# Performance work log

Hardware: AMD Instinct MI355X
Metric: run time of the kernel (lower is better)

## Reference

```python
import jax, jax.numpy as jnp
import numpy as np

N, E, F_IN, H, R = 50000, 1600000, 770, 64, 3


def _lin_params(key, fan_in, fan_out, scale=0.02):
    return jax.random.normal(key, (fan_in, fan_out), dtype=jnp.float32) * scale


def setup_inputs() -> dict:
    key = jax.random.key(0)
    ks = jax.random.split(key, 20)
    x = jax.random.normal(ks[0], (N, F_IN), dtype=jnp.float32)
    edge_index = jax.random.randint(ks[1], (2, E), 0, N, dtype=jnp.int64)
    edge_type = jax.random.randint(ks[2], (E,), 0, R, dtype=jnp.int64)
    # RGCN layer params: W [R, fin, H], root [fin, H], bias [H]
    W1 = jax.random.normal(ks[3], (R, F_IN, H), dtype=jnp.float32) * 0.02
    root1 = _lin_params(ks[4], F_IN, H)
    b1 = jnp.zeros((H,), jnp.float32)
    W2 = jax.random.normal(ks[5], (R, H, H), dtype=jnp.float32) * 0.02
    root2 = _lin_params(ks[6], H, H)
    b2 = jnp.zeros((H,), jnp.float32)
    W3 = jax.random.normal(ks[7], (R, H, H), dtype=jnp.float32) * 0.02
    root3 = _lin_params(ks[8], H, H)
    b3 = jnp.zeros((H,), jnp.float32)
    ln_g = jnp.ones((H,), jnp.float32)
    ln_b = jnp.zeros((H,), jnp.float32)
    ew1 = _lin_params(ks[9], 2 * H, H)
    eb1 = jnp.zeros((H,), jnp.float32)
    ew2 = _lin_params(ks[10], H, 3)
    eb2 = jnp.zeros((3,), jnp.float32)
    nw1 = _lin_params(ks[11], H, H // 2)
    nb1 = jnp.zeros((H // 2,), jnp.float32)
    nw2 = _lin_params(ks[12], H // 2, 2)
    nb2 = jnp.zeros((2,), jnp.float32)
    return dict(x=x, edge_index=edge_index, edge_type=edge_type,
                W1=W1, root1=root1, b1=b1, W2=W2, root2=root2, b2=b2,
                W3=W3, root3=root3, b3=b3, ln_g=ln_g, ln_b=ln_b,
                ew1=ew1, eb1=eb1, ew2=ew2, eb2=eb2,
                nw1=nw1, nb1=nb1, nw2=nw2, nb2=nb2)


def rgcn_conv(x, W, root, bias, row, col, etype):
    # per-relation transform of all nodes: [R, N, H]
    xr = jnp.einsum('nf,rfh->rnh', x, W)
    msg = xr[etype, row]                       # [E, H] gather
    seg = etype * N + col                      # combined (relation, dst) key
    sums = jax.ops.segment_sum(msg, seg, num_segments=R * N)
    cnt = jax.ops.segment_sum(jnp.ones((msg.shape[0],), msg.dtype), seg,
                              num_segments=R * N)
    mean = sums / jnp.maximum(cnt, 1.0)[:, None]   # mean aggr per relation
    agg = mean.reshape(R, N, -1).sum(0)
    return agg + x @ root + bias


def layer_norm(x, g, b, eps=1e-5):
    mu = x.mean(-1, keepdims=True)
    var = ((x - mu) ** 2).mean(-1, keepdims=True)
    return (x - mu) * jax.lax.rsqrt(var + eps) * g + b


def reference(x, edge_index, edge_type, W1, root1, b1, W2, root2, b2,
              W3, root3, b3, ln_g, ln_b, ew1, eb1, ew2, eb2,
              nw1, nb1, nw2, nb2):
    row, col = edge_index[0], edge_index[1]
    x1 = jax.nn.relu(rgcn_conv(x, W1, root1, b1, row, col, edge_type))
    x2 = jax.nn.relu(rgcn_conv(x1, W2, root2, b2, row, col, edge_type))
    x3 = layer_norm(rgcn_conv(x2, W3, root3, b3, row, col, edge_type), ln_g, ln_b)
    # edge classifier on concatenated endpoint features (dropout = identity in eval)
    ef = jnp.concatenate([x3[row], x3[col]], axis=-1)    # [E, 2H]
    eh = jax.nn.relu(ef @ ew1 + eb1)
    edge_out = jax.nn.log_softmax(eh @ ew2 + eb2, axis=-1)
    nh = jax.nn.relu(x3 @ nw1 + nb1)
    node_out = jax.nn.log_softmax(nh @ nw2 + nb2, axis=-1)
    return edge_out, node_out
```

## Files before the change

kernel.cpp:

```cpp
#include <hip/hip_runtime.h>
#include <hip/hip_bf16.h>
#include <math.h>

#define Nn 50000
#define Ee 1600000
#define RR 3
#define RN (RR * Nn)
#define FIN 770
#define KPAD1 800

typedef __attribute__((ext_vector_type(8))) short short8;
typedef __attribute__((ext_vector_type(4))) float floatx4;

static __device__ __forceinline__ unsigned short f2bf(float v) {
  __hip_bfloat16 h = __float2bfloat16(v);
  return *(unsigned short*)&h;
}

__global__ __launch_bounds__(256) void count_kernel(const int* __restrict__ ei,
                                                    const int* __restrict__ et,
                                                    int* __restrict__ counts,
                                                    int* __restrict__ rank) {
  int e = blockIdx.x * 256 + threadIdx.x;
  if (e >= Ee) return;
  int col = ei[Ee + e];
  int r = et[e];
  rank[e] = atomicAdd(&counts[r * Nn + col], 1);
}

__global__ __launch_bounds__(256) void scan1_kernel(const int* __restrict__ counts,
                                                    int* __restrict__ offs,
                                                    int* __restrict__ bsums, int n) {
  __shared__ int sh[256];
  int t = threadIdx.x;
  int base = blockIdx.x * 1024 + t * 4;
  int v0 = (base + 0 < n) ? counts[base + 0] : 0;
  int v1 = (base + 1 < n) ? counts[base + 1] : 0;
  int v2 = (base + 2 < n) ? counts[base + 2] : 0;
  int v3 = (base + 3 < n) ? counts[base + 3] : 0;
  int tot = v0 + v1 + v2 + v3;
  sh[t] = tot;
  __syncthreads();
  for (int off = 1; off < 256; off <<= 1) {
    int v = (t >= off) ? sh[t - off] : 0;
    __syncthreads();
    sh[t] += v;
    __syncthreads();
  }
  int run = sh[t] - tot;
  if (base + 0 < n) offs[base + 0] = run; run += v0;
  if (base + 1 < n) offs[base + 1] = run; run += v1;
  if (base + 2 < n) offs[base + 2] = run; run += v2;
  if (base + 3 < n) offs[base + 3] = run;
  if (t == 255) bsums[blockIdx.x] = sh[255];
}

__global__ __launch_bounds__(256) void scan_top_kernel(int* __restrict__ bsums, int nb) {
  __shared__ int sh[256];
  int t = threadIdx.x;
  int v = (t < nb) ? bsums[t] : 0;
  sh[t] = v;
  __syncthreads();
  for (int off = 1; off < 256; off <<= 1) {
    int x = (t >= off) ? sh[t - off] : 0;
    __syncthreads();
    sh[t] += x;
    __syncthreads();
  }
  if (t < nb) bsums[t] = sh[t] - v;
}

__global__ __launch_bounds__(256) void scan_add_kernel(int* __restrict__ offs,
                                                       const int* __restrict__ bsums,
                                                       int n) {
  int i = blockIdx.x * 256 + threadIdx.x;
  if (i > n) return;
  if (i == n) { offs[n] = Ee; return; }
  offs[i] += bsums[i >> 10];
}

__global__ __launch_bounds__(256) void fill_kernel(const int* __restrict__ ei,
                                                   const int* __restrict__ et,
                                                   const int* __restrict__ offs,
                                                   const int* __restrict__ rank,
                                                   int* __restrict__ srcs) {
  int e = blockIdx.x * 256 + threadIdx.x;
  if (e >= Ee) return;
  int row = ei[e];
  int col = ei[Ee + e];
  int r = et[e];
  int s = r * Nn + col;
  srcs[offs[s] + rank[e]] = row;
}

__global__ __launch_bounds__(256) void prep_wt_kernel(const float* __restrict__ W,
                                                      const float* __restrict__ root,
                                                      unsigned short* __restrict__ Wt,
                                                      int K, int Kpad) {
  int i = blockIdx.x * 256 + threadIdx.x;
  if (i >= 256 * Kpad) return;
  int c = i / Kpad, k = i % Kpad;
  float v = 0.f;
  if (k < K) {
    if (c < 192) {
      int r = c >> 6, h = c & 63;
      v = W[((long)r * K + k) * 64 + h];
    } else {
      v = root[k * 64 + (c - 192)];
    }
  }
  Wt[i] = f2bf(v);
}

__global__ __launch_bounds__(256) void prep_wth_kernel(const float* __restrict__ ew1,
                                                       const float* __restrict__ eb1,
                                                       unsigned short* __restrict__ Wth,
                                                       float* __restrict__ biasH) {
  int i = blockIdx.x * 256 + threadIdx.x;
  if (i < 128) biasH[i] = (i < 64) ? eb1[i] : 0.f;
  if (i >= 256 * 64) return;
  int c = i >> 6, k = i & 63;
  float v = 0.f;
  if (c < 64) v = ew1[k * 64 + c];
  else if (c < 128) v = ew1[(64 + k) * 64 + (c - 64)];
  Wth[i] = f2bf(v);
}

#define ASTR 40
#define BSTR 40

#define LOAD_A_FULL(k0)                                        \
  {                                                            \
    const float* ap = aRow + (k0) + ac;                        \
    a01 = *(const float4*)(ap + 0);                            \
    a23 = *(const float4*)(ap + 4);                            \
  }
#define LOAD_A_MASK(k0)                                        \
  {                                                            \
    int kb = (k0) + ac;                                        \
    a01.x = (rowOK && kb + 0 < K) ? aRow[kb + 0] : 0.f;        \
    a01.y = (rowOK && kb + 1 < K) ? aRow[kb + 1] : 0.f;        \
    a01.z = (rowOK && kb + 2 < K) ? aRow[kb + 2] : 0.f;        \
    a01.w = (rowOK && kb + 3 < K) ? aRow[kb + 3] : 0.f;        \
    a23.x = (rowOK && kb + 4 < K) ? aRow[kb + 4] : 0.f;        \
    a23.y = (rowOK && kb + 5 < K) ? aRow[kb + 5] : 0.f;        \
    a23.z = (rowOK && kb + 6 < K) ? aRow[kb + 6] : 0.f;        \
    a23.w = (rowOK && kb + 7 < K) ? aRow[kb + 7] : 0.f;        \
  }
#define LOAD_A(k0)                                                   \
  {                                                                  \
    if (aBf16) { aB = *(const int4*)(aRowB + (k0) + ac); }           \
    else if (rowOK && (k0) + 32 <= K) LOAD_A_FULL(k0)                \
    else LOAD_A_MASK(k0)                                             \
  }
#define LOAD_B(k0)                                             \
  {                                                            \
    b0 = *(const int4*)(wRow + (k0));                          \
  }
#define STORE_TILE()                                                          \
  {                                                                           \
    if (aBf16) {                                                              \
      *(int4*)&As[ar * ASTR + ac] = aB;                                       \
    } else {                                                                  \
      __hip_bfloat162* adst = (__hip_bfloat162*)&As[ar * ASTR + ac];          \
      adst[0] = __hip_bfloat162(__float2bfloat16(a01.x), __float2bfloat16(a01.y)); \
      adst[1] = __hip_bfloat162(__float2bfloat16(a01.z), __float2bfloat16(a01.w)); \
      adst[2] = __hip_bfloat162(__float2bfloat16(a23.x), __float2bfloat16(a23.y)); \
      adst[3] = __hip_bfloat162(__float2bfloat16(a23.z), __float2bfloat16(a23.w)); \
    }                                                                         \
    *(int4*)&Bs[br * BSTR + bo] = b0;                                         \
  }

__global__ __launch_bounds__(1024) void gemm_bf16_kernel(
    const void* __restrict__ Ag, const unsigned short* __restrict__ Wt,
    unsigned short* __restrict__ Cg, const float* __restrict__ bias,
    int M, int K, int Kpad, int Ncol, int aBf16) {
  __shared__ unsigned short As[256 * ASTR];
  __shared__ unsigned short Bs[256 * BSTR];
  int t = threadIdx.x;
  int lane = t & 63;
  int wid = t >> 6;
  int quad = lane >> 4;
  int l16 = lane & 15;
  int rowBase = blockIdx.x * 256;
  int mbase = (wid >> 2) * 64;
  int nbase = (wid & 3) * 64;

  floatx4 acc[4][4];
#pragma unroll
  for (int i = 0; i < 4; ++i)
#pragma unroll
    for (int j = 0; j < 4; ++j) acc[i][j] = (floatx4){0.f, 0.f, 0.f, 0.f};

  int ar = t >> 2;
  int ac = (t & 3) * 8;
  long gm = rowBase + ar;
  bool rowOK = (gm < M);
  const float* aRow = (const float*)Ag + gm * (long)K;
  const unsigned short* aRowB = (const unsigned short*)Ag + gm * (long)K;
  int br = t >> 2;
  int bo = (t & 3) * 8;
  const unsigned short* wRow = Wt + (size_t)br * Kpad + bo;

  float4 a01, a23;
  int4 aB;
  int4 b0;

  int KT = Kpad / 32;
  LOAD_A(0);
  LOAD_B(0);

  for (int kt = 0; kt < KT; ++kt) {
    STORE_TILE();
    __syncthreads();

    if (kt + 1 < KT) {
      int k0n = (kt + 1) * 32;
      LOAD_A(k0n);
      LOAD_B(k0n);
    }

    short8 af[4], bfr[4];
#pragma unroll
    for (int i = 0; i < 4; ++i)
      af[i] = *(const short8*)&As[(mbase + i * 16 + l16) * ASTR + quad * 8];
#pragma unroll
    for (int j = 0; j < 4; ++j)
      bfr[j] = *(const short8*)&Bs[(nbase + j * 16 + l16) * BSTR + quad * 8];

#pragma unroll
    for (int i = 0; i < 4; ++i)
#pragma unroll
      for (int j = 0; j < 4; ++j)
        acc[i][j] = __builtin_amdgcn_mfma_f32_16x16x32_bf16(af[i], bfr[j], acc[i][j], 0, 0, 0);
    __syncthreads();
  }

#pragma unroll
  for (int j = 0; j < 4; ++j) {
    int gn = nbase + j * 16 + l16;
    if (gn >= Ncol) continue;
    float bv = bias ? bias[gn] : 0.f;
#pragma unroll
    for (int i = 0; i < 4; ++i) {
      int gm0 = rowBase + mbase + i * 16 + quad * 4;
#pragma unroll
      for (int r = 0; r < 4; ++r) {
        int gmm = gm0 + r;
        if (gmm < M) Cg[(long)gmm * Ncol + gn] = f2bf(acc[i][j][r] + bv);
      }
    }
  }
}

#define AGG_RESOLVE(ii, ee, vv, rr)                                   \
  {                                                                   \
    if ((ii) < c0)       { ee = b0 + (ii);         vv = inv0; rr = 0; }   \
    else if ((ii) < c01) { ee = b1 + ((ii) - c0);  vv = inv1; rr = 64; }  \
    else                 { ee = b2 + ((ii) - c01); vv = inv2; rr = 128; } \
  }
#define AGG_FMA8(v, inv)                                              \
  {                                                                   \
    unsigned u0 = (unsigned)v.x, u1 = (unsigned)v.y;                  \
    unsigned u2 = (unsigned)v.z, u3 = (unsigned)v.w;                  \
    a0 = fmaf(__int_as_float(u0 << 16), inv, a0);                     \
    a1 = fmaf(__int_as_float(u0 & 0xffff0000u), inv, a1);             \
    a2 = fmaf(__int_as_float(u1 << 16), inv, a2);                     \
    a3 = fmaf(__int_as_float(u1 & 0xffff0000u), inv, a3);             \
    a4 = fmaf(__int_as_float(u2 << 16), inv, a4);                     \
    a5 = fmaf(__int_as_float(u2 & 0xffff0000u), inv, a5);             \
    a6 = fmaf(__int_as_float(u3 << 16), inv, a6);                     \
    a7 = fmaf(__int_as_float(u3 & 0xffff0000u), inv, a7);             \
  }

__global__ __launch_bounds__(256) void agg_kernel(const unsigned short* __restrict__ XR,
                                                  const int* __restrict__ offs,
                                                  const int* __restrict__ srcs,
                                                  const float* __restrict__ bias,
                                                  const float* __restrict__ lng,
                                                  const float* __restrict__ lnb,
                                                  float* __restrict__ out, int mode) {
  int lane = threadIdx.x & 63;
  int wid = threadIdx.x >> 6;
  int slot = lane >> 3;
  int l8 = lane & 7;
  int dst = blockIdx.x * 4 + wid;
  if (dst >= Nn) return;

  int b0 = offs[dst],          e0 = offs[dst + 1];
  int b1 = offs[Nn + dst],     e1 = offs[Nn + dst + 1];
  int b2 = offs[2 * Nn + dst], e2 = offs[2 * Nn + dst + 1];
  int c0 = e0 - b0, c1 = e1 - b1, c2 = e2 - b2;
  int c01 = c0 + c1;
  int tot = c01 + c2;
  float inv0 = (c0 > 0) ? 1.f / (float)c0 : 0.f;
  float inv1 = (c1 > 0) ? 1.f / (float)c1 : 0.f;
  float inv2 = (c2 > 0) ? 1.f / (float)c2 : 0.f;

  float a0 = 0.f, a1 = 0.f, a2 = 0.f, a3 = 0.f;
  float a4 = 0.f, a5 = 0.f, a6 = 0.f, a7 = 0.f;
  for (int i = slot; i < tot; i += 16) {
    int ea; float iva; int ra;
    AGG_RESOLVE(i, ea, iva, ra);
    int ib = i + 8;
    int eb; float ivb; int rb;
    if (ib < tot) { AGG_RESOLVE(ib, eb, ivb, rb); }
    else          { eb = ea; ivb = 0.f; rb = ra; }
    int sa = srcs[ea];
    int sb = srcs[eb];
    int4 va = *(const int4*)&XR[(long)sa * 256 + ra + l8 * 8];
    int4 vb = *(const int4*)&XR[(long)sb * 256 + rb + l8 * 8];
    AGG_FMA8(va, iva);
    AGG_FMA8(vb, ivb);
  }
#pragma unroll
  for (int m = 8; m < 64; m <<= 1) {
    a0 += __shfl_xor(a0, m, 64); a1 += __shfl_xor(a1, m, 64);
    a2 += __shfl_xor(a2, m, 64); a3 += __shfl_xor(a3, m, 64);
    a4 += __shfl_xor(a4, m, 64); a5 += __shfl_xor(a5, m, 64);
    a6 += __shfl_xor(a6, m, 64); a7 += __shfl_xor(a7, m, 64);
  }

  int4 rt = *(const int4*)&XR[(long)dst * 256 + 192 + l8 * 8];
  unsigned r0 = (unsigned)rt.x, r1 = (unsigned)rt.y;
  unsigned r2 = (unsigned)rt.z, r3 = (unsigned)rt.w;
  float4 bv0 = *(const float4*)&bias[l8 * 8];
  float4 bv1 = *(const float4*)&bias[l8 * 8 + 4];
  float t0 = a0 + __int_as_float(r0 << 16) + bv0.x;
  float t1 = a1 + __int_as_float(r0 & 0xffff0000u) + bv0.y;
  float t2 = a2 + __int_as_float(r1 << 16) + bv0.z;
  float t3 = a3 + __int_as_float(r1 & 0xffff0000u) + bv0.w;
  float t4 = a4 + __int_as_float(r2 << 16) + bv1.x;
  float t5 = a5 + __int_as_float(r2 & 0xffff0000u) + bv1.y;
  float t6 = a6 + __int_as_float(r3 << 16) + bv1.z;
  float t7 = a7 + __int_as_float(r3 & 0xffff0000u) + bv1.w;

  if (mode == 0) {
    if (slot == 0) {
      unsigned short* outB = (unsigned short*)out;
      int4 o;
      o.x = (int)((unsigned)f2bf(fmaxf(t0, 0.f)) | ((unsigned)f2bf(fmaxf(t1, 0.f)) << 16));
      o.y = (int)((unsigned)f2bf(fmaxf(t2, 0.f)) | ((unsigned)f2bf(fmaxf(t3, 0.f)) << 16));
      o.z = (int)((unsigned)f2bf(fmaxf(t4, 0.f)) | ((unsigned)f2bf(fmaxf(t5, 0.f)) << 16));
      o.w = (int)((unsigned)f2bf(fmaxf(t6, 0.f)) | ((unsigned)f2bf(fmaxf(t7, 0.f)) << 16));
      *(int4*)&outB[(long)dst * 64 + l8 * 8] = o;
    }
  } else {
    float s = t0 + t1 + t2 + t3 + t4 + t5 + t6 + t7;
    s += __shfl_xor(s, 1, 64); s += __shfl_xor(s, 2, 64); s += __shfl_xor(s, 4, 64);
    float mu = s * (1.f / 64.f);
    float d0 = t0 - mu, d1 = t1 - mu, d2 = t2 - mu, d3 = t3 - mu;
    float d4 = t4 - mu, d5 = t5 - mu, d6 = t6 - mu, d7 = t7 - mu;
    float vv = d0 * d0 + d1 * d1 + d2 * d2 + d3 * d3 +
               d4 * d4 + d5 * d5 + d6 * d6 + d7 * d7;
    vv += __shfl_xor(vv, 1, 64); vv += __shfl_xor(vv, 2, 64); vv += __shfl_xor(vv, 4, 64);
    float rstd = rsqrtf(vv * (1.f / 64.f) + 1e-5f);
    if (slot == 0) {
      float4 g0 = *(const float4*)&lng[l8 * 8];
      float4 g1 = *(const float4*)&lng[l8 * 8 + 4];
      float4 c0v = *(const float4*)&lnb[l8 * 8];
      float4 c1v = *(const float4*)&lnb[l8 * 8 + 4];
      float4 o0, o1;
      o0.x = d0 * rstd * g0.x + c0v.x;
      o0.y = d1 * rstd * g0.y + c0v.y;
      o0.z = d2 * rstd * g0.z + c0v.z;
      o0.w = d3 * rstd * g0.w + c0v.w;
      o1.x = d4 * rstd * g1.x + c1v.x;
      o1.y = d5 * rstd * g1.y + c1v.y;
      o1.z = d6 * rstd * g1.z + c1v.z;
      o1.w = d7 * rstd * g1.w + c1v.w;
      *(float4*)&out[(long)dst * 64 + l8 * 8] = o0;
      *(float4*)&out[(long)dst * 64 + l8 * 8 + 4] = o1;
    }
  }
}

__global__ __launch_bounds__(256) void edge_head_kernel(const unsigned short* __restrict__ AB,
                                                        const int* __restrict__ ei,
                                                        const float* __restrict__ ew2,
                                                        const float* __restrict__ eb2,
                                                        float* __restrict__ out) {
  int t = threadIdx.x;
  long e = (long)blockIdx.x * 32 + (t >> 3);
  if (e >= Ee) return;
  int sub = t & 7;
  int row = ei[e];
  int col = ei[Ee + e];
  int4 av = *(const int4*)&AB[(long)row * 128 + sub * 8];
  int4 bv = *(const int4*)&AB[(long)col * 128 + 64 + sub * 8];
  float acc0 = 0.f, acc1 = 0.f, acc2 = 0.f;
  const int* ad = (const int*)&av;
  const int* bd = (const int*)&bv;
#pragma unroll
  for (int d = 0; d < 4; ++d) {
    int A = ad[d], B = bd[d];
    float a0 = __int_as_float(A << 16);
    float a1 = __int_as_float(A & 0xffff0000);
    float b0 = __int_as_float(B << 16);
    float b1 = __int_as_float(B & 0xffff0000);
    float e0 = fmaxf(a0 + b0, 0.f);
    float e1 = fmaxf(a1 + b1, 0.f);
    int h = sub * 8 + d * 2;
    acc0 = fmaf(e0, ew2[h * 3 + 0], acc0);
    acc1 = fmaf(e0, ew2[h * 3 + 1], acc1);
    acc2 = fmaf(e0, ew2[h * 3 + 2], acc2);
    acc0 = fmaf(e1, ew2[h * 3 + 3], acc0);
    acc1 = fmaf(e1, ew2[h * 3 + 4], acc1);
    acc2 = fmaf(e1, ew2[h * 3 + 5], acc2);
  }
  acc0 += __shfl_xor(acc0, 1, 64); acc0 += __shfl_xor(acc0, 2, 64); acc0 += __shfl_xor(acc0, 4, 64);
  acc1 += __shfl_xor(acc1, 1, 64); acc1 += __shfl_xor(acc1, 2, 64); acc1 += __shfl_xor(acc1, 4, 64);
  acc2 += __shfl_xor(acc2, 1, 64); acc2 += __shfl_xor(acc2, 2, 64); acc2 += __shfl_xor(acc2, 4, 64);
  if (sub == 0) {
    float l0 = acc0 + eb2[0], l1 = acc1 + eb2[1], l2 = acc2 + eb2[2];
    float mx = fmaxf(l0, fmaxf(l1, l2));
    float ls = mx + logf(expf(l0 - mx) + expf(l1 - mx) + expf(l2 - mx));
    out[e * 3 + 0] = l0 - ls;
    out[e * 3 + 1] = l1 - ls;
    out[e * 3 + 2] = l2 - ls;
  }
}

__global__ __launch_bounds__(256) void node_head_kernel(const float* __restrict__ x3,
                                                        const float* __restrict__ nw1,
                                                        const float* __restrict__ nb1,
                                                        const float* __restrict__ nw2,
                                                        const float* __restrict__ nb2,
                                                        float* __restrict__ out) {
  __shared__ float w1s[64 * 32];
  __shared__ float w2s[64];
  for (int i = threadIdx.x; i < 2048; i += 256) w1s[i] = nw1[i];
  if (threadIdx.x < 64) w2s[threadIdx.x] = nw2[threadIdx.x];
  __syncthreads();
  int n = blockIdx.x * 256 + threadIdx.x;
  if (n >= Nn) return;
  float acc[32];
#pragma unroll
  for (int c = 0; c < 32; ++c) acc[c] = nb1[c];
  for (int k = 0; k < 64; ++k) {
    float xv = x3[(long)n * 64 + k];
#pragma unroll
    for (int c = 0; c < 32; ++c) acc[c] += xv * w1s[k * 32 + c];
  }
  float l0 = nb2[0], l1 = nb2[1];
#pragma unroll
  for (int c = 0; c < 32; ++c) {
    float h = fmaxf(acc[c], 0.f);
    l0 += h * w2s[c * 2 + 0];
    l1 += h * w2s[c * 2 + 1];
  }
  float mx = fmaxf(l0, l1);
  float ls = mx + logf(expf(l0 - mx) + expf(l1 - mx));
  out[(long)3 * Ee + (long)n * 2 + 0] = l0 - ls;
  out[(long)3 * Ee + (long)n * 2 + 1] = l1 - ls;
}

extern "C" void kernel_launch(void* const* d_in, const int* in_sizes, int n_in,
                              void* d_out, int out_size, void* d_ws, size_t ws_size,
                              hipStream_t stream) {
  const float* x = (const float*)d_in[0];
  const int* ei = (const int*)d_in[1];
  const int* et = (const int*)d_in[2];
  const float* W1 = (const float*)d_in[3];
  const float* root1 = (const float*)d_in[4];
  const float* b1 = (const float*)d_in[5];
  const float* W2 = (const float*)d_in[6];
  const float* root2 = (const float*)d_in[7];
  const float* b2 = (const float*)d_in[8];
  const float* W3 = (const float*)d_in[9];
  const float* root3 = (const float*)d_in[10];
  const float* b3 = (const float*)d_in[11];
  const float* lng = (const float*)d_in[12];
  const float* lnb = (const float*)d_in[13];
  const float* ew1 = (const float*)d_in[14];
  const float* eb1 = (const float*)d_in[15];
  const float* ew2 = (const float*)d_in[16];
  const float* eb2 = (const float*)d_in[17];
  const float* nw1 = (const float*)d_in[18];
  const float* nb1 = (const float*)d_in[19];
  const float* nw2 = (const float*)d_in[20];
  const float* nb2 = (const float*)d_in[21];
  float* out = (float*)d_out;

  char* p = (char*)d_ws;
  size_t off = 0;
  auto alloc = [&](size_t bytes) {
    void* r = p + off;
    off += (bytes + 255) & ~(size_t)255;
    return r;
  };
  unsigned short* XR = (unsigned short*)alloc((size_t)Nn * 256 * 2);
  float* xA = (float*)alloc((size_t)Nn * 64 * 4);
  float* xB = (float*)alloc((size_t)Nn * 64 * 4);
  int* srcs = (int*)alloc((size_t)Ee * 4);
  int* offs = (int*)alloc((size_t)(RN + 1) * 4);
  int* bsums = (int*)alloc(1024);
  unsigned short* Wt1 = (unsigned short*)alloc((size_t)256 * KPAD1 * 2);
  unsigned short* Wt2 = (unsigned short*)alloc((size_t)256 * 64 * 2);
  unsigned short* Wt3 = (unsigned short*)alloc((size_t)256 * 64 * 2);
  unsigned short* Wth = (unsigned short*)alloc((size_t)256 * 64 * 2);
  float* biasH = (float*)alloc(128 * 4);
  int* rank = (int*)xA;
  int* counts = (int*)xB;

  int nb = (RN + 1023) / 1024;

  hipMemsetAsync(counts, 0, (size_t)RN * 4, stream);
  count_kernel<<<(Ee + 255) / 256, 256, 0, stream>>>(ei, et, counts, rank);
  scan1_kernel<<<nb, 256, 0, stream>>>(counts, offs, bsums, RN);
  scan_top_kernel<<<1, 256, 0, stream>>>(bsums, nb);
  scan_add_kernel<<<(RN + 256) / 256 + 1, 256, 0, stream>>>(offs, bsums, RN);
  fill_kernel<<<(Ee + 255) / 256, 256, 0, stream>>>(ei, et, offs, rank, srcs);

  prep_wt_kernel<<<(256 * KPAD1 + 255) / 256, 256, 0, stream>>>(W1, root1, Wt1, FIN, KPAD1);
  prep_wt_kernel<<<(256 * 64 + 255) / 256, 256, 0, stream>>>(W2, root2, Wt2, 64, 64);
  prep_wt_kernel<<<(256 * 64 + 255) / 256, 256, 0, stream>>>(W3, root3, Wt3, 64, 64);
  prep_wth_kernel<<<(256 * 64 + 255) / 256, 256, 0, stream>>>(ew1, eb1, Wth, biasH);

  int gemmBlocks = (Nn + 255) / 256;
  int aggBlocks = (Nn + 3) / 4;

  gemm_bf16_kernel<<<gemmBlocks, 1024, 0, stream>>>(x, Wt1, XR, nullptr, Nn, FIN, KPAD1, 256, 0);
  agg_kernel<<<aggBlocks, 256, 0, stream>>>(XR, offs, srcs, b1, nullptr, nullptr, xA, 0);
  gemm_bf16_kernel<<<gemmBlocks, 1024, 0, stream>>>(xA, Wt2, XR, nullptr, Nn, 64, 64, 256, 1);
  agg_kernel<<<aggBlocks, 256, 0, stream>>>(XR, offs, srcs, b2, nullptr, nullptr, xB, 0);
  gemm_bf16_kernel<<<gemmBlocks, 1024, 0, stream>>>(xB, Wt3, XR, nullptr, Nn, 64, 64, 256, 1);
  agg_kernel<<<aggBlocks, 256, 0, stream>>>(XR, offs, srcs, b3, lng, lnb, xA, 1);
  gemm_bf16_kernel<<<gemmBlocks, 1024, 0, stream>>>(xA, Wth, XR, biasH, Nn, 64, 64, 128, 0);
  edge_head_kernel<<<(Ee + 31) / 32, 256, 0, stream>>>(XR, ei, ew2, eb2, out);
  node_head_kernel<<<(Nn + 255) / 256, 256, 0, stream>>>(xA, nw1, nb1, nw2, nb2, out);
}
```

Before: 665.2 us.

## Co-launch edge counting with layer-1 GEMM and node head with head GEMM

Folds the edge-count atomics into extra blocks of the first GEMM launch and the node-head MLP into extra blocks of the edge-head projection GEMM, so independent work shares a launch and fills idle CUs. The layer-3 aggregation now also writes a bf16 copy of x3, so the head GEMM reads half the bytes. Weight prep is moved ahead of counting. Fewer launches and better overlap, at the cost of heterogeneous blocks inside one 1024-thread kernel and extra LDS use from the node-head shared arrays.

```diff
diff --git a/kernel.cpp b/kernel.cpp
--- a/kernel.cpp
+++ b/kernel.cpp
@@ -15,17 +15,6 @@
 static __device__ __forceinline__ unsigned short f2bf(float v) {
   __hip_bfloat16 h = __float2bfloat16(v);
   return *(unsigned short*)&h;
-}
-
-__global__ __launch_bounds__(256) void count_kernel(const int* __restrict__ ei,
-                                                    const int* __restrict__ et,
-                                                    int* __restrict__ counts,
-                                                    int* __restrict__ rank) {
-  int e = blockIdx.x * 256 + threadIdx.x;
-  if (e >= Ee) return;
-  int col = ei[Ee + e];
-  int r = et[e];
-  rank[e] = atomicAdd(&counts[r * Nn + col], 1);
 }
 
 __global__ __launch_bounds__(256) void scan1_kernel(const int* __restrict__ counts,
@@ -171,86 +160,137 @@
     *(int4*)&Bs[br * BSTR + bo] = b0;                                         \
   }
 
+#define GEMM_CORE(GBIDX)                                                      \
+  __shared__ unsigned short As[256 * ASTR];                                   \
+  __shared__ unsigned short Bs[256 * BSTR];                                   \
+  int t = threadIdx.x;                                                        \
+  int lane = t & 63;                                                          \
+  int wid = t >> 6;                                                           \
+  int quad = lane >> 4;                                                       \
+  int l16 = lane & 15;                                                        \
+  int rowBase = (GBIDX) * 256;                                                \
+  int mbase = (wid >> 2) * 64;                                                \
+  int nbase = (wid & 3) * 64;                                                 \
+  floatx4 acc[4][4];                                                          \
+  _Pragma("unroll")                                                           \
+  for (int i = 0; i < 4; ++i)                                                 \
+    _Pragma("unroll")                                                         \
+    for (int j = 0; j < 4; ++j) acc[i][j] = (floatx4){0.f, 0.f, 0.f, 0.f};    \
+  int ar = t >> 2;                                                            \
+  int ac = (t & 3) * 8;                                                       \
+  long gm = rowBase + ar;                                                     \
+  bool rowOK = (gm < M);                                                      \
+  const float* aRow = (const float*)Ag + gm * (long)K;                        \
+  const unsigned short* aRowB = (const unsigned short*)Ag + gm * (long)K;     \
+  int br = t >> 2;                                                            \
+  int bo = (t & 3) * 8;                                                       \
+  const unsigned short* wRow = Wt + (size_t)br * Kpad + bo;                   \
+  float4 a01, a23;                                                            \
+  int4 aB;                                                                    \
+  int4 b0;                                                                    \
+  int KT = Kpad / 32;                                                         \
+  LOAD_A(0);                                                                  \
+  LOAD_B(0);                                                                  \
+  for (int kt = 0; kt < KT; ++kt) {                                           \
+    STORE_TILE();                                                             \
+    __syncthreads();                                                          \
+    if (kt + 1 < KT) {                                                        \
+      int k0n = (kt + 1) * 32;                                                \
+      LOAD_A(k0n);                                                            \
+      LOAD_B(k0n);                                                            \
+    }                                                                         \
+    short8 af[4], bfr[4];                                                     \
+    _Pragma("unroll")                                                         \
+    for (int i = 0; i < 4; ++i)                                               \
+      af[i] = *(const short8*)&As[(mbase + i * 16 + l16) * ASTR + quad * 8];  \
+    _Pragma("unroll")                                                         \
+    for (int j = 0; j < 4; ++j)                                               \
+      bfr[j] = *(const short8*)&Bs[(nbase + j * 16 + l16) * BSTR + quad * 8]; \
+    _Pragma("unroll")                                                         \
+    for (int i = 0; i < 4; ++i)                                               \
+      _Pragma("unroll")                                                       \
+      for (int j = 0; j < 4; ++j)                                             \
+        acc[i][j] = __builtin_amdgcn_mfma_f32_16x16x32_bf16(af[i], bfr[j], acc[i][j], 0, 0, 0); \
+    __syncthreads();                                                          \
+  }                                                                           \
+  _Pragma("unroll")                                                           \
+  for (int j = 0; j < 4; ++j) {                                               \
+    int gn = nbase + j * 16 + l16;                                            \
+    if (gn >= Ncol) continue;                                                 \
+    float bv = bias ? bias[gn] : 0.f;                                         \
+    _Pragma("unroll")                                                         \
+    for (int i = 0; i < 4; ++i) {                                             \
+      int gm0 = rowBase + mbase + i * 16 + quad * 4;                          \
+      _Pragma("unroll")                                                       \
+      for (int r = 0; r < 4; ++r) {                                           \
+        int gmm = gm0 + r;                                                    \
+        if (gmm < M) Cg[(long)gmm * Ncol + gn] = f2bf(acc[i][j][r] + bv);     \
+      }                                                                       \
+    }                                                                         \
+  }
+
 __global__ __launch_bounds__(1024) void gemm_bf16_kernel(
     const void* __restrict__ Ag, const unsigned short* __restrict__ Wt,
     unsigned short* __restrict__ Cg, const float* __restrict__ bias,
     int M, int K, int Kpad, int Ncol, int aBf16) {
-  __shared__ unsigned short As[256 * ASTR];
-  __shared__ unsigned short Bs[256 * BSTR];
-  int t = threadIdx.x;
-  int lane = t & 63;
-  int wid = t >> 6;
-  int quad = lane >> 4;
-  int l16 = lane & 15;
-  int rowBase = blockIdx.x * 256;
-  int mbase = (wid >> 2) * 64;
-  int nbase = (wid & 3) * 64;
-
-  floatx4 acc[4][4];
+  GEMM_CORE(blockIdx.x)
+}
+
+__global__ __launch_bounds__(1024) void gemm_count_kernel(
+    const void* __restrict__ Ag, const unsigned short* __restrict__ Wt,
+    unsigned short* __restrict__ Cg, const float* __restrict__ bias,
+    int M, int K, int Kpad, int Ncol, int aBf16, int gemmBlocks,
+    const int* __restrict__ ei, const int* __restrict__ et,
+    int* __restrict__ counts, int* __restrict__ rank) {
+  if ((int)blockIdx.x >= gemmBlocks) {
+    long e = (long)(blockIdx.x - gemmBlocks) * 1024 + threadIdx.x;
+    if (e < Ee) {
+      int col = ei[Ee + e];
+      int r = et[e];
+      rank[e] = atomicAdd(&counts[r * Nn + col], 1);
+    }
+    return;
+  }
+  GEMM_CORE(blockIdx.x)
+}
+
+__global__ __launch_bounds__(1024) void gemm_nh_kernel(
+    const void* __restrict__ Ag, const unsigned short* __restrict__ Wt,
+    unsigned short* __restrict__ Cg, const float* __restrict__ bias,
+    int M, int K, int Kpad, int Ncol, int aBf16, int gemmBlocks,
+    const float* __restrict__ x3, const float* __restrict__ nw1,
+    const float* __restrict__ nb1, const float* __restrict__ nw2,
+    const float* __restrict__ nb2, float* __restrict__ outN) {
+  if ((int)blockIdx.x >= gemmBlocks) {
+    __shared__ float w1s[64 * 32];
+    __shared__ float w2s[64];
+    for (int i = threadIdx.x; i < 2048; i += 1024) w1s[i] = nw1[i];
+    if (threadIdx.x < 64) w2s[threadIdx.x] = nw2[threadIdx.x];
+    __syncthreads();
+    int n = (blockIdx.x - gemmBlocks) * 1024 + threadIdx.x;
+    if (n >= Nn) return;
+    float accv[32];
 #pragma unroll
-  for (int i = 0; i < 4; ++i)
+    for (int c = 0; c < 32; ++c) accv[c] = nb1[c];
+    for (int k = 0; k < 64; ++k) {
+      float xv = x3[(long)n * 64 + k];
 #pragma unroll
-    for (int j = 0; j < 4; ++j) acc[i][j] = (floatx4){0.f, 0.f, 0.f, 0.f};
-
-  int ar = t >> 2;
-  int ac = (t & 3) * 8;
-  long gm = rowBase + ar;
-  bool rowOK = (gm < M);
-  const float* aRow = (const float*)Ag + gm * (long)K;
-  const unsigned short* aRowB = (const unsigned short*)Ag + gm * (long)K;
-  int br = t >> 2;
-  int bo = (t & 3) * 8;
-  const unsigned short* wRow = Wt + (size_t)br * Kpad + bo;
-
-  float4 a01, a23;
-  int4 aB;
-  int4 b0;
-
-  int KT = Kpad / 32;
-  LOAD_A(0);
-  LOAD_B(0);
-
-  for (int kt = 0; kt < KT; ++kt) {
-    STORE_TILE();
-    __syncthreads();
-
-    if (kt + 1 < KT) {
-      int k0n = (kt + 1) * 32;
-      LOAD_A(k0n);
-      LOAD_B(k0n);
+      for (int c = 0; c < 32; ++c) accv[c] += xv * w1s[k * 32 + c];
     }
-
-    short8 af[4], bfr[4];
+    float l0 = nb2[0], l1 = nb2[1];
 #pragma unroll
-    for (int i = 0; i < 4; ++i)
-      af[i] = *(const short8*)&As[(mbase + i * 16 + l16) * ASTR + quad * 8];
-#pragma unroll
-    for (int j = 0; j < 4; ++j)
-      bfr[j] = *(const short8*)&Bs[(nbase + j * 16 + l16) * BSTR + quad * 8];
-
-#pragma unroll
-    for (int i = 0; i < 4; ++i)
-#pragma unroll
-      for (int j = 0; j < 4; ++j)
-        acc[i][j] = __builtin_amdgcn_mfma_f32_16x16x32_bf16(af[i], bfr[j], acc[i][j], 0, 0, 0);
-    __syncthreads();
-  }
-
-#pragma unroll
-  for (int j = 0; j < 4; ++j) {
-    int gn = nbase + j * 16 + l16;
-    if (gn >= Ncol) continue;
-    float bv = bias ? bias[gn] : 0.f;
-#pragma unroll
-    for (int i = 0; i < 4; ++i) {
-      int gm0 = rowBase + mbase + i * 16 + quad * 4;
-#pragma unroll
-      for (int r = 0; r < 4; ++r) {
-        int gmm = gm0 + r;
-        if (gmm < M) Cg[(long)gmm * Ncol + gn] = f2bf(acc[i][j][r] + bv);
-      }
+    for (int c = 0; c < 32; ++c) {
+      float h = fmaxf(accv[c], 0.f);
+      l0 += h * w2s[c * 2 + 0];
+      l1 += h * w2s[c * 2 + 1];
     }
-  }
+    float mx = fmaxf(l0, l1);
+    float ls = mx + logf(expf(l0 - mx) + expf(l1 - mx));
+    outN[(long)3 * Ee + (long)n * 2 + 0] = l0 - ls;
+    outN[(long)3 * Ee + (long)n * 2 + 1] = l1 - ls;
+    return;
+  }
+  GEMM_CORE(blockIdx.x)
 }
 
 #define AGG_RESOLVE(ii, ee, vv, rr)                                   \
@@ -279,7 +319,9 @@
                                                   const float* __restrict__ bias,
                                                   const float* __restrict__ lng,
                                                   const float* __restrict__ lnb,
-                                                  float* __restrict__ out, int mode) {
+                                                  float* __restrict__ out,
+                                                  unsigned short* __restrict__ outh,
+                                                  int mode) {
   int lane = threadIdx.x & 63;
   int wid = threadIdx.x >> 6;
   int slot = lane >> 3;
@@ -371,6 +413,14 @@
       o1.w = d7 * rstd * g1.w + c1v.w;
       *(float4*)&out[(long)dst * 64 + l8 * 8] = o0;
       *(float4*)&out[(long)dst * 64 + l8 * 8 + 4] = o1;
+      if (outh) {
+        int4 oh;
+        oh.x = (int)((unsigned)f2bf(o0.x) | ((unsigned)f2bf(o0.y) << 16));
+        oh.y = (int)((unsigned)f2bf(o0.z) | ((unsigned)f2bf(o0.w) << 16));
+        oh.z = (int)((unsigned)f2bf(o1.x) | ((unsigned)f2bf(o1.y) << 16));
+        oh.w = (int)((unsigned)f2bf(o1.z) | ((unsigned)f2bf(o1.w) << 16));
+        *(int4*)&outh[(long)dst * 64 + l8 * 8] = oh;
+      }
     }
   }
 }
@@ -421,40 +471,6 @@
   }
 }
 
-__global__ __launch_bounds__(256) void node_head_kernel(const float* __restrict__ x3,
-                                                        const float* __restrict__ nw1,
-                                                        const float* __restrict__ nb1,
-                                                        const float* __restrict__ nw2,
-                                                        const float* __restrict__ nb2,
-                                                        float* __restrict__ out) {
-  __shared__ float w1s[64 * 32];
-  __shared__ float w2s[64];
-  for (int i = threadIdx.x; i < 2048; i += 256) w1s[i] = nw1[i];
-  if (threadIdx.x < 64) w2s[threadIdx.x] = nw2[threadIdx.x];
-  __syncthreads();
-  int n = blockIdx.x * 256 + threadIdx.x;
-  if (n >= Nn) return;
-  float acc[32];
-#pragma unroll
-  for (int c = 0; c < 32; ++c) acc[c] = nb1[c];
-  for (int k = 0; k < 64; ++k) {
-    float xv = x3[(long)n * 64 + k];
-#pragma unroll
-    for (int c = 0; c < 32; ++c) acc[c] += xv * w1s[k * 32 + c];
-  }
-  float l0 = nb2[0], l1 = nb2[1];
-#pragma unroll
-  for (int c = 0; c < 32; ++c) {
-    float h = fmaxf(acc[c], 0.f);
-    l0 += h * w2s[c * 2 + 0];
-    l1 += h * w2s[c * 2 + 1];
-  }
-  float mx = fmaxf(l0, l1);
-  float ls = mx + logf(expf(l0 - mx) + expf(l1 - mx));
-  out[(long)3 * Ee + (long)n * 2 + 0] = l0 - ls;
-  out[(long)3 * Ee + (long)n * 2 + 1] = l1 - ls;
-}
-
 extern "C" void kernel_launch(void* const* d_in, const int* in_sizes, int n_in,
                               void* d_out, int out_size, void* d_ws, size_t ws_size,
                               hipStream_t stream) {
@@ -502,31 +518,35 @@
   float* biasH = (float*)alloc(128 * 4);
   int* rank = (int*)xA;
   int* counts = (int*)xB;
+  unsigned short* xh = (unsigned short*)xB;
 
   int nb = (RN + 1023) / 1024;
-
+  int gemmBlocks = (Nn + 255) / 256;
+  int aggBlocks = (Nn + 3) / 4;
+  int countBlocks = (Ee + 1023) / 1024;
+  int nhBlocks = (Nn + 1023) / 1024;
+
+  prep_wt_kernel<<<(256 * KPAD1 + 255) / 256, 256, 0, stream>>>(W1, root1, Wt1, FIN, KPAD1);
+  prep_wt_kernel<<<(256 * 64 + 255) / 256, 256, 0, stream>>>(W2, root2, Wt2, 64, 64);
+  prep_wt_kernel<<<(256 * 64 + 255) / 256, 256, 0, stream>>>(W3, root3, Wt3, 64, 64);
+  prep_wth_kernel<<<(256 * 64 + 255) / 256, 256, 0, stream>>>(ew1, eb1, Wth, biasH);
   hipMemsetAsync(counts, 0, (size_t)RN * 4, stream);
-  count_kernel<<<(Ee + 255) / 256, 256, 0, stream>>>(ei, et, counts, rank);
+
+  gemm_count_kernel<<<gemmBlocks + countBlocks, 1024, 0, stream>>>(
+      x, Wt1, XR, nullptr, Nn, FIN, KPAD1, 256, 0, gemmBlocks, ei, et, counts, rank);
+
   scan1_kernel<<<nb, 256, 0, stream>>>(counts, offs, bsums, RN);
   scan_top_kernel<<<1, 256, 0, stream>>>(bsums, nb);
   scan_add_kernel<<<(RN + 256) / 256 + 1, 256, 0, stream>>>(offs, bsums, RN);
   fill_kernel<<<(Ee + 255) / 256, 256, 0, stream>>>(ei, et, offs, rank, srcs);
 
-  prep_wt_kernel<<<(256 * KPAD1 + 255) / 256, 256, 0, stream>>>(W1, root1, Wt1, FIN, KPAD1);
-  prep_wt_kernel<<<(256 * 64 + 255) / 256, 256, 0, stream>>>(W2, root2, Wt2, 64, 64);
-  prep_wt_kernel<<<(256 * 64 + 255) / 256, 256, 0, stream>>>(W3, root3, Wt3, 64, 64);
-  prep_wth_kernel<<<(256 * 64 + 255) / 256, 256, 0, stream>>>(ew1, eb1, Wth, biasH);
-
-  int gemmBlocks = (Nn + 255) / 256;
-  int aggBlocks = (Nn + 3) / 4;
-
-  gemm_bf16_kernel<<<gemmBlocks, 1024, 0, stream>>>(x, Wt1, XR, nullptr, Nn, FIN, KPAD1, 256, 0);
-  agg_kernel<<<aggBlocks, 256, 0, stream>>>(XR, offs, srcs, b1, nullptr, nullptr, xA, 0);
+  agg_kernel<<<aggBlocks, 256, 0, stream>>>(XR, offs, srcs, b1, nullptr, nullptr, xA, nullptr, 0);
   gemm_bf16_kernel<<<gemmBlocks, 1024, 0, stream>>>(xA, Wt2, XR, nullptr, Nn, 64, 64, 256, 1);
-  agg_kernel<<<aggBlocks, 256, 0, stream>>>(XR, offs, srcs, b2, nullptr, nullptr, xB, 0);
+  agg_kernel<<<aggBlocks, 256, 0, stream>>>(XR, offs, srcs, b2, nullptr, nullptr, xB, nullptr, 0);
   gemm_bf16_kernel<<<gemmBlocks, 1024, 0, stream>>>(xB, Wt3, XR, nullptr, Nn, 64, 64, 256, 1);
-  agg_kernel<<<aggBlocks, 256, 0, stream>>>(XR, offs, srcs, b3, lng, lnb, xA, 1);
-  gemm_bf16_kernel<<<gemmBlocks, 1024, 0, stream>>>(xA, Wth, XR, biasH, Nn, 64, 64, 128, 0);
+  agg_kernel<<<aggBlocks, 256, 0, stream>>>(XR, offs, srcs, b3, lng, lnb, xA, xh, 1);
+  gemm_nh_kernel<<<gemmBlocks + nhBlocks, 1024, 0, stream>>>(
+      xh, Wth, XR, biasH, Nn, 64, 64, 128, 1, gemmBlocks,
+      xA, nw1, nb1, nw2, nb2, out);
   edge_head_kernel<<<(Ee + 31) / 32, 256, 0, stream>>>(XR, ei, ew2, eb2, out);
-  node_head_kernel<<<(Nn + 255) / 256, 256, 0, stream>>>(xA, nw1, nb1, nw2, nb2, out);
-}
+}
```

Result: faster. 622.7 us (-6.4%).
